# Kernel tuning notes

Measured on AMD Instinct MI355X. Metric: run time of the kernel, lower is better.

Reference implementation:

```python
import jax, jax.numpy as jnp
import numpy as np

NUM_HEADS = 8
QK_DIM = 64
V_DIM = 64


def _conv1x1(W, b, x):
    # W: [out, in], x: [N, in, T, V] -> [N, out, T, V]
    return jnp.einsum('oc,nctv->notv', W, x) + b[None, :, None, None]


def setup_inputs() -> dict:
    key = jax.random.key(0)
    ks = jax.random.split(key, 10)
    N, C, T, V = 8, 256, 1024, 25
    s = 0.02
    return {
        'feature': jax.random.normal(ks[0], (N, C, T, V), jnp.float32),
        'text_feature': jax.random.normal(ks[1], (1, 512, 1, V), jnp.float32),
        'Wq': jax.random.normal(ks[2], (NUM_HEADS * QK_DIM, 512), jnp.float32) * s,
        'bq': jax.random.normal(ks[3], (NUM_HEADS * QK_DIM,), jnp.float32) * s,
        'Wk': jax.random.normal(ks[4], (NUM_HEADS * QK_DIM, 512), jnp.float32) * s,
        'bk': jax.random.normal(ks[5], (NUM_HEADS * QK_DIM,), jnp.float32) * s,
        'Wv': jax.random.normal(ks[6], (V_DIM, C), jnp.float32) * s,
        'bv': jax.random.normal(ks[7], (V_DIM,), jnp.float32) * s,
        'Wo': jax.random.normal(ks[8], (C, NUM_HEADS * V_DIM), jnp.float32) * s,
        'bo': jax.random.normal(ks[9], (C,), jnp.float32) * s,
    }


def reference(feature, text_feature, Wq, bq, Wk, bk, Wv, bv, Wo, bo):
    N, C, T, V = feature.shape
    tf = jnp.broadcast_to(text_feature, (N, 512, 1, V))  # expand over batch
    # Q/K from text features (T dim collapses to 1)
    q = _conv1x1(Wq, bq, tf).reshape(N, NUM_HEADS, QK_DIM, V)
    k = _conv1x1(Wk, bk, tf).reshape(N, NUM_HEADS, QK_DIM, V)
    v = _conv1x1(Wv, bv, feature)  # [N, v_dim, T, V]
    energy = jnp.einsum('nhcu,nhcv->nhuv', q, k) / jnp.sqrt(jnp.float32(QK_DIM))
    attn = jax.nn.softmax(energy, axis=-1)  # [N, H, V, V]
    z = jnp.einsum('nctu,nhuv->nhctv', v, attn).reshape(N, NUM_HEADS * V_DIM, T, V)
    out = _conv1x1(Wo, bo, z) + feature
    return out
```

## Files before the change

kernel.cpp:

```cpp
#include <hip/hip_runtime.h>
#include <hip/hip_bf16.h>


typedef __attribute__((ext_vector_type(8))) short short8;
typedef __attribute__((ext_vector_type(4))) short short4v;
typedef __attribute__((ext_vector_type(4))) float f4v;

static __device__ __forceinline__ unsigned short f2bf(float f) {
  union { float f; unsigned u; } v; v.f = f;
  unsigned r = v.u + 0x7fffu + ((v.u >> 16) & 1u);
  return (unsigned short)(r >> 16);
}
static __device__ __forceinline__ float bf2f(unsigned short h) {
  union { unsigned u; float f; } v; v.u = ((unsigned)h) << 16;
  return v.f;
}


__global__ void k_qk_conv(const float* __restrict__ tf,
                          const float* __restrict__ Wq, const float* __restrict__ bq,
                          const float* __restrict__ Wk, const float* __restrict__ bk,
                          const float* __restrict__ Wv, const float* __restrict__ Wo,
                          unsigned short* __restrict__ WvP,
                          unsigned short* __restrict__ WoP,
                          float* __restrict__ qkP)
{
  __shared__ float tfl[12800];
  const int b = blockIdx.x, tid = threadIdx.x;
  if (b < 100) {
    for (int i = tid; i < 12800; i += 256) tfl[i] = tf[i];
    __syncthreads();
    int idx = b * 256 + tid;
    int isK = idx >= 12800;
    int j = isK ? idx - 12800 : idx;
    int g = j / 25, u = j - 25 * g;
    const float* wrow = (isK ? Wk : Wq) + g * 512;
    float s = (isK ? bk : bq)[g];
    for (int i = 0; i < 512; ++i) s += wrow[i] * tfl[i * 25 + u];
    qkP[idx] = s;
  } else {
    int cb = b - 100;
    for (int i = cb * 256 + tid; i < 16384; i += 64 * 256) {
      WvP[i] = f2bf(Wv[i]);
    }
    for (int i = cb * 256 + tid; i < 131072; i += 64 * 256) {
      WoP[i] = f2bf(Wo[i]);
    }
  }
}

__global__ void k_attn(const float* __restrict__ qkP,
                       unsigned short* __restrict__ attnP)
{
  __shared__ float ql[1600], kl[1600], attl[625];
  const int h = blockIdx.x, tid = threadIdx.x;
  for (int i = tid; i < 1600; i += 256) {
    ql[i] = qkP[h * 1600 + i];
    kl[i] = qkP[12800 + h * 1600 + i];
  }
  __syncthreads();
  if (tid < 25) {
    int u = tid;
    float e[25];
    float mx = -1e30f;
    #pragma unroll
    for (int v = 0; v < 25; ++v) {
      float s = 0.f;
      #pragma unroll
      for (int r = 0; r < 64; ++r) s += ql[r * 25 + u] * kl[r * 25 + v];
      s *= 0.125f;
      e[v] = s;
      mx = fmaxf(mx, s);
    }
    float den = 0.f;
    #pragma unroll
    for (int v = 0; v < 25; ++v) { e[v] = __expf(e[v] - mx); den += e[v]; }
    float inv = 1.f / den;
    #pragma unroll
    for (int v = 0; v < 25; ++v) attl[u * 25 + v] = e[v] * inv;
  }
  __syncthreads();
  for (int i = tid; i < 1280; i += 256) {
    int vp = i / 40, u = i - 40 * vp;
    attnP[h * 1280 + i] =
        (vp < 25 && u < 25) ? f2bf(attl[u * 25 + vp]) : (unsigned short)0;
  }
}

__launch_bounds__(512, 4)
__global__ void k_main(const float* __restrict__ feature,
                       const float* __restrict__ bv,
                       const float* __restrict__ bo,
                       const unsigned short* __restrict__ WvP,
                       const unsigned short* __restrict__ WoP,
                       const unsigned short* __restrict__ attnP,
                       float* __restrict__ out)
{
  extern __shared__ char smem[];
  unsigned short* Fl = (unsigned short*)smem;
  unsigned short* Zl = (unsigned short*)smem;
  unsigned short* Vl = (unsigned short*)(smem + 66560);

  const int tid  = threadIdx.x;
  const int wave = tid >> 6;
  const int lane = tid & 63;
  const int quad = lane >> 4;
  const int l16  = lane & 15;
  const int n  = blockIdx.x & 7;
  const int tb = blockIdx.x >> 3;
  const int t0 = tb * 2;

  if (tid < 462) {
    short8 z = {0, 0, 0, 0, 0, 0, 0, 0};
    int pc = tid / 33, off = tid - 33 * pc;
    int t = pc / 7, vp = 25 + (pc - 7 * t);
    *reinterpret_cast<short8*>(&Fl[(t * 32 + vp) * 264 + off * 8]) = z;
  }

  {
    const int c = tid >> 1, p = tid & 1;
    const float2* src = reinterpret_cast<const float2*>(
        feature + ((size_t)(n * 256 + c) * 1024 + t0) * 25);
    for (int i = p; i < 25; i += 2) {
      float2 f = src[i];
      int j0 = 2 * i;
      {
        int j = j0;       int t = (j >= 25); int vp = j - 25 * t;
        Fl[(t * 32 + vp) * 264 + c] = f2bf(f.x);
      }
      {
        int j = j0 + 1;   int t = (j >= 25); int vp = j - 25 * t;
        Fl[(t * 32 + vp) * 264 + c] = f2bf(f.y);
      }
    }
  }

  const int mt1 = wave & 3, nh1 = wave >> 2;
  short8 wa[8];
  #pragma unroll
  for (int ks = 0; ks < 8; ++ks)
    wa[ks] = *reinterpret_cast<const short8*>(
        WvP + (mt1 * 16 + l16) * 256 + ks * 32 + quad * 8);

  __syncthreads();

  f4v acc[2][4];
  #pragma unroll
  for (int mi = 0; mi < 2; ++mi) {
    const int o0 = wave * 32 + mi * 16 + quad * 4;
    float bo4[4];
    #pragma unroll
    for (int r = 0; r < 4; ++r) bo4[r] = bo[o0 + r];
    #pragma unroll
    for (int ni = 0; ni < 4; ++ni) {
      short4v fr = *reinterpret_cast<const short4v*>(
          &Fl[(ni * 16 + l16) * 264 + o0]);
      #pragma unroll
      for (int r = 0; r < 4; ++r)
        acc[mi][ni][r] = bo4[r] + bf2f((unsigned short)fr[r]);
    }
  }

  {
    f4v accv[2];
    #pragma unroll
    for (int ni = 0; ni < 2; ++ni) {
      #pragma unroll
      for (int r = 0; r < 4; ++r) accv[ni][r] = bv[mt1 * 16 + quad * 4 + r];
    }
    #pragma unroll
    for (int ks = 0; ks < 8; ++ks) {
      #pragma unroll
      for (int ni = 0; ni < 2; ++ni) {
        int colb = (2 * nh1 + ni) * 16 + l16;
        short8 b = *reinterpret_cast<const short8*>(
            &Fl[colb * 264 + ks * 32 + quad * 8]);
        accv[ni] = __builtin_amdgcn_mfma_f32_16x16x32_bf16(wa[ks], b, accv[ni], 0, 0, 0);
      }
    }
    #pragma unroll
    for (int ni = 0; ni < 2; ++ni) {
      int colb = (2 * nh1 + ni) * 16 + l16;
      #pragma unroll
      for (int r = 0; r < 4; ++r) {
        int c = mt1 * 16 + quad * 4 + r;
        Vl[c * 72 + colb] = f2bf(accv[ni][r]);
      }
    }
  }

  const int t2 = wave >> 2, q2 = wave & 3;
  short8 ab[4];
  #pragma unroll
  for (int nj = 0; nj < 4; ++nj) {
    int h = 2 * q2 + (nj >> 1), vph = nj & 1;
    ab[nj] = *reinterpret_cast<const short8*>(
        attnP + h * 1280 + (vph * 16 + l16) * 40 + quad * 8);
  }

  __syncthreads();

  #pragma unroll
  for (int mi = 0; mi < 4; ++mi) {
    short8 a = *reinterpret_cast<const short8*>(
        &Vl[(mi * 16 + l16) * 72 + t2 * 32 + quad * 8]);
    #pragma unroll
    for (int nj = 0; nj < 4; ++nj) {
      f4v z = {0.f, 0.f, 0.f, 0.f};
      f4v accz = __builtin_amdgcn_mfma_f32_16x16x32_bf16(a, ab[nj], z, 0, 0, 0);
      int h = 2 * q2 + (nj >> 1), vph = nj & 1;
      int col = t2 * 32 + vph * 16 + l16;
      int k0 = h * 64 + mi * 16 + quad * 4;
      short4v zz;
      #pragma unroll
      for (int r = 0; r < 4; ++r) zz[r] = (short)f2bf(accz[r]);
      *reinterpret_cast<short4v*>(&Zl[col * 520 + k0]) = zz;
    }
  }

  short8 af01[2][2];
  #pragma unroll
  for (int pk = 0; pk < 2; ++pk)
    #pragma unroll
    for (int mi = 0; mi < 2; ++mi)
      af01[pk][mi] = *reinterpret_cast<const short8*>(
          WoP + (wave * 32 + mi * 16 + l16) * 512 + pk * 32 + quad * 8);

  __syncthreads();

  #pragma unroll
  for (int ks = 0; ks < 16; ++ks) {
    short8 bfr[4], afr[2];
    #pragma unroll
    for (int ni = 0; ni < 4; ++ni)
      bfr[ni] = *reinterpret_cast<const short8*>(
          &Zl[(ni * 16 + l16) * 520 + ks * 32 + quad * 8]);
    if (ks < 2) {
      afr[0] = af01[ks][0];
      afr[1] = af01[ks][1];
    } else {
      #pragma unroll
      for (int mi = 0; mi < 2; ++mi)
        afr[mi] = *reinterpret_cast<const short8*>(
            WoP + (wave * 32 + mi * 16 + l16) * 512 + ks * 32 + quad * 8);
    }
    #pragma unroll
    for (int mi = 0; mi < 2; ++mi) {
      #pragma unroll
      for (int ni = 0; ni < 4; ++ni)
        acc[mi][ni] =
            __builtin_amdgcn_mfma_f32_16x16x32_bf16(afr[mi], bfr[ni], acc[mi][ni], 0, 0, 0);
    }
  }

  #pragma unroll
  for (int ni = 0; ni < 4; ++ni) {
    int colb = ni * 16 + l16;
    int t = colb >> 5, vp = colb & 31;
    if (vp < 25) {
      #pragma unroll
      for (int mi = 0; mi < 2; ++mi) {
        #pragma unroll
        for (int r = 0; r < 4; ++r) {
          int o = wave * 32 + mi * 16 + quad * 4 + r;
          out[((size_t)(n * 256 + o) * 1024 + (t0 + t)) * 25 + vp] = acc[mi][ni][r];
        }
      }
    }
  }
}

extern "C" void kernel_launch(void* const* d_in, const int* in_sizes, int n_in,
                              void* d_out, int out_size, void* d_ws, size_t ws_size,
                              hipStream_t stream)
{
  const float* feature = (const float*)d_in[0];
  const float* tf      = (const float*)d_in[1];
  const float* Wq      = (const float*)d_in[2];
  const float* bq      = (const float*)d_in[3];
  const float* Wk      = (const float*)d_in[4];
  const float* bk      = (const float*)d_in[5];
  const float* Wv      = (const float*)d_in[6];
  const float* bv      = (const float*)d_in[7];
  const float* Wo      = (const float*)d_in[8];
  const float* bo      = (const float*)d_in[9];
  float* out = (float*)d_out;

  unsigned short* WvP   = (unsigned short*)d_ws;
  unsigned short* WoP   = WvP + 16384;
  unsigned short* attnP = WoP + 131072;
  float* qkP = (float*)(attnP + 10240);

  hipLaunchKernelGGL(k_qk_conv, dim3(164), dim3(256), 0, stream,
                     tf, Wq, bq, Wk, bk, Wv, Wo, WvP, WoP, qkP);
  hipLaunchKernelGGL(k_attn, dim3(8), dim3(256), 0, stream, qkP, attnP);

  hipFuncSetAttribute(reinterpret_cast<const void*>(&k_main),
                      hipFuncAttributeMaxDynamicSharedMemorySize, 75776);
  hipLaunchKernelGGL(k_main, dim3(4096), dim3(512), 75776, stream,
                     feature, bv, bo, WvP, WoP, attnP, out);
}
```

Measured before the change: 547.7 us.

## Make main kernel loop over time chunks with double-buffered feature prefetch

The main kernel now launches 256 workgroups, each looping over 16 two-frame tiles of one batch instead of one tile per workgroup. The next tile's feature data is prefetched into registers while the current tile is computed, then written into an alternate LDS buffer. The full Wo fragment set is held in registers for the whole loop rather than reloaded per tile, and outputs use nontemporal stores. In exchange, LDS grows to about 140 KB so only one workgroup fits per CU, the launch bound drops to 2, and register pressure rises, all of which cut the number of waves available to hide latency.

```diff
diff --git a/kernel.cpp b/kernel.cpp
--- a/kernel.cpp
+++ b/kernel.cpp
@@ -87,7 +87,7 @@
   }
 }
 
-__launch_bounds__(512, 4)
+__launch_bounds__(512, 2)
 __global__ void k_main(const float* __restrict__ feature,
                        const float* __restrict__ bv,
                        const float* __restrict__ bo,
@@ -97,43 +97,30 @@
                        float* __restrict__ out)
 {
   extern __shared__ char smem[];
-  unsigned short* Fl = (unsigned short*)smem;
-  unsigned short* Zl = (unsigned short*)smem;
-  unsigned short* Vl = (unsigned short*)(smem + 66560);
+  unsigned short* FlA = (unsigned short*)smem;
+  unsigned short* FlB = (unsigned short*)(smem + 33792);
+  unsigned short* Vl  = (unsigned short*)(smem + 67584);
+  unsigned short* Zl  = (unsigned short*)(smem + 76800);
 
   const int tid  = threadIdx.x;
   const int wave = tid >> 6;
   const int lane = tid & 63;
   const int quad = lane >> 4;
   const int l16  = lane & 15;
-  const int n  = blockIdx.x & 7;
-  const int tb = blockIdx.x >> 3;
-  const int t0 = tb * 2;
-
-  if (tid < 462) {
-    short8 z = {0, 0, 0, 0, 0, 0, 0, 0};
-    int pc = tid / 33, off = tid - 33 * pc;
-    int t = pc / 7, vp = 25 + (pc - 7 * t);
-    *reinterpret_cast<short8*>(&Fl[(t * 32 + vp) * 264 + off * 8]) = z;
-  }
-
-  {
-    const int c = tid >> 1, p = tid & 1;
-    const float2* src = reinterpret_cast<const float2*>(
-        feature + ((size_t)(n * 256 + c) * 1024 + t0) * 25);
-    for (int i = p; i < 25; i += 2) {
-      float2 f = src[i];
-      int j0 = 2 * i;
-      {
-        int j = j0;       int t = (j >= 25); int vp = j - 25 * t;
-        Fl[(t * 32 + vp) * 264 + c] = f2bf(f.x);
-      }
-      {
-        int j = j0 + 1;   int t = (j >= 25); int vp = j - 25 * t;
-        Fl[(t * 32 + vp) * 264 + c] = f2bf(f.y);
-      }
-    }
-  }
+  const int wg    = blockIdx.x;
+  const int n     = wg >> 5;
+  const int chunk = wg & 31;
+
+  const int c = tid >> 1, p = tid & 1;
+  const size_t rowbase = ((size_t)(n * 256 + c) * 1024) * 25;
+
+  short8 wo[2][16];
+  #pragma unroll
+  for (int mi = 0; mi < 2; ++mi)
+    #pragma unroll
+    for (int ks = 0; ks < 16; ++ks)
+      wo[mi][ks] = *reinterpret_cast<const short8*>(
+          WoP + (wave * 32 + mi * 16 + l16) * 512 + ks * 32 + quad * 8);
 
   const int mt1 = wave & 3, nh1 = wave >> 2;
   short8 wa[8];
@@ -141,53 +128,6 @@
   for (int ks = 0; ks < 8; ++ks)
     wa[ks] = *reinterpret_cast<const short8*>(
         WvP + (mt1 * 16 + l16) * 256 + ks * 32 + quad * 8);
-
-  __syncthreads();
-
-  f4v acc[2][4];
-  #pragma unroll
-  for (int mi = 0; mi < 2; ++mi) {
-    const int o0 = wave * 32 + mi * 16 + quad * 4;
-    float bo4[4];
-    #pragma unroll
-    for (int r = 0; r < 4; ++r) bo4[r] = bo[o0 + r];
-    #pragma unroll
-    for (int ni = 0; ni < 4; ++ni) {
-      short4v fr = *reinterpret_cast<const short4v*>(
-          &Fl[(ni * 16 + l16) * 264 + o0]);
-      #pragma unroll
-      for (int r = 0; r < 4; ++r)
-        acc[mi][ni][r] = bo4[r] + bf2f((unsigned short)fr[r]);
-    }
-  }
-
-  {
-    f4v accv[2];
-    #pragma unroll
-    for (int ni = 0; ni < 2; ++ni) {
-      #pragma unroll
-      for (int r = 0; r < 4; ++r) accv[ni][r] = bv[mt1 * 16 + quad * 4 + r];
-    }
-    #pragma unroll
-    for (int ks = 0; ks < 8; ++ks) {
-      #pragma unroll
-      for (int ni = 0; ni < 2; ++ni) {
-        int colb = (2 * nh1 + ni) * 16 + l16;
-        short8 b = *reinterpret_cast<const short8*>(
-            &Fl[colb * 264 + ks * 32 + quad * 8]);
-        accv[ni] = __builtin_amdgcn_mfma_f32_16x16x32_bf16(wa[ks], b, accv[ni], 0, 0, 0);
-      }
-    }
-    #pragma unroll
-    for (int ni = 0; ni < 2; ++ni) {
-      int colb = (2 * nh1 + ni) * 16 + l16;
-      #pragma unroll
-      for (int r = 0; r < 4; ++r) {
-        int c = mt1 * 16 + quad * 4 + r;
-        Vl[c * 72 + colb] = f2bf(accv[ni][r]);
-      }
-    }
-  }
 
   const int t2 = wave >> 2, q2 = wave & 3;
   short8 ab[4];
@@ -198,75 +138,161 @@
         attnP + h * 1280 + (vph * 16 + l16) * 40 + quad * 8);
   }
 
+  float bo4[2][4];
+  #pragma unroll
+  for (int mi = 0; mi < 2; ++mi)
+    #pragma unroll
+    for (int r = 0; r < 4; ++r) bo4[mi][r] = bo[wave * 32 + mi * 16 + quad * 4 + r];
+  float bvv[4];
+  #pragma unroll
+  for (int r = 0; r < 4; ++r) bvv[r] = bv[mt1 * 16 + quad * 4 + r];
+
+  {
+    short8 z = {0, 0, 0, 0, 0, 0, 0, 0};
+    for (int i = tid; i < 924; i += 512) {
+      int pc = i / 33, off = i - 33 * pc;
+      unsigned short* F = (pc < 14) ? FlA : FlB;
+      int r = (pc < 14) ? pc : pc - 14;
+      int t = r / 7, vp = 25 + (r - 7 * t);
+      *reinterpret_cast<short8*>(&F[(t * 32 + vp) * 264 + off * 8]) = z;
+    }
+  }
+
+  float2 fn[13];
+  {
+    const float2* s2 = reinterpret_cast<const float2*>(
+        feature + rowbase + (size_t)(chunk * 32) * 25);
+    #pragma unroll
+    for (int j = 0; j < 13; ++j) { int i = p + 2 * j; if (i < 25) fn[j] = s2[i]; }
+  }
+  #pragma unroll
+  for (int j = 0; j < 13; ++j) {
+    int i = p + 2 * j;
+    if (i < 25) {
+      int j0 = 2 * i;
+      { int jj = j0;     int t = (jj >= 25); int vp = jj - 25 * t; FlA[(t*32+vp)*264 + c] = f2bf(fn[j].x); }
+      { int jj = j0 + 1; int t = (jj >= 25); int vp = jj - 25 * t; FlA[(t*32+vp)*264 + c] = f2bf(fn[j].y); }
+    }
+  }
   __syncthreads();
 
-  #pragma unroll
-  for (int mi = 0; mi < 4; ++mi) {
-    short8 a = *reinterpret_cast<const short8*>(
-        &Vl[(mi * 16 + l16) * 72 + t2 * 32 + quad * 8]);
-    #pragma unroll
-    for (int nj = 0; nj < 4; ++nj) {
-      f4v z = {0.f, 0.f, 0.f, 0.f};
-      f4v accz = __builtin_amdgcn_mfma_f32_16x16x32_bf16(a, ab[nj], z, 0, 0, 0);
-      int h = 2 * q2 + (nj >> 1), vph = nj & 1;
-      int col = t2 * 32 + vph * 16 + l16;
-      int k0 = h * 64 + mi * 16 + quad * 4;
-      short4v zz;
-      #pragma unroll
-      for (int r = 0; r < 4; ++r) zz[r] = (short)f2bf(accz[r]);
-      *reinterpret_cast<short4v*>(&Zl[col * 520 + k0]) = zz;
-    }
-  }
-
-  short8 af01[2][2];
-  #pragma unroll
-  for (int pk = 0; pk < 2; ++pk)
-    #pragma unroll
-    for (int mi = 0; mi < 2; ++mi)
-      af01[pk][mi] = *reinterpret_cast<const short8*>(
-          WoP + (wave * 32 + mi * 16 + l16) * 512 + pk * 32 + quad * 8);
-
-  __syncthreads();
-
-  #pragma unroll
-  for (int ks = 0; ks < 16; ++ks) {
-    short8 bfr[4], afr[2];
-    #pragma unroll
-    for (int ni = 0; ni < 4; ++ni)
-      bfr[ni] = *reinterpret_cast<const short8*>(
-          &Zl[(ni * 16 + l16) * 520 + ks * 32 + quad * 8]);
-    if (ks < 2) {
-      afr[0] = af01[ks][0];
-      afr[1] = af01[ks][1];
-    } else {
+  #pragma unroll 1
+  for (int it = 0; it < 16; ++it) {
+    unsigned short* Fc  = (it & 1) ? FlB : FlA;
+    unsigned short* Fnx = (it & 1) ? FlA : FlB;
+    const int t0 = chunk * 32 + it * 2;
+
+    if (it < 15) {
+      const float2* s2 = reinterpret_cast<const float2*>(
+          feature + rowbase + (size_t)(t0 + 2) * 25);
+      #pragma unroll
+      for (int j = 0; j < 13; ++j) { int i = p + 2 * j; if (i < 25) fn[j] = s2[i]; }
+      __builtin_amdgcn_sched_barrier(0);
+    }
+
+    f4v acc[2][4];
+    #pragma unroll
+    for (int mi = 0; mi < 2; ++mi) {
+      const int o0 = wave * 32 + mi * 16 + quad * 4;
+      #pragma unroll
+      for (int ni = 0; ni < 4; ++ni) {
+        short4v fr = *reinterpret_cast<const short4v*>(&Fc[(ni * 16 + l16) * 264 + o0]);
+        #pragma unroll
+        for (int r = 0; r < 4; ++r)
+          acc[mi][ni][r] = bo4[mi][r] + bf2f((unsigned short)fr[r]);
+      }
+    }
+
+    {
+      f4v accv[2];
+      #pragma unroll
+      for (int ni = 0; ni < 2; ++ni)
+        #pragma unroll
+        for (int r = 0; r < 4; ++r) accv[ni][r] = bvv[r];
+      #pragma unroll
+      for (int ks = 0; ks < 8; ++ks) {
+        #pragma unroll
+        for (int ni = 0; ni < 2; ++ni) {
+          int colb = (2 * nh1 + ni) * 16 + l16;
+          short8 b = *reinterpret_cast<const short8*>(&Fc[colb * 264 + ks * 32 + quad * 8]);
+          accv[ni] = __builtin_amdgcn_mfma_f32_16x16x32_bf16(wa[ks], b, accv[ni], 0, 0, 0);
+        }
+      }
+      #pragma unroll
+      for (int ni = 0; ni < 2; ++ni) {
+        int colb = (2 * nh1 + ni) * 16 + l16;
+        #pragma unroll
+        for (int r = 0; r < 4; ++r) {
+          int cc = mt1 * 16 + quad * 4 + r;
+          Vl[cc * 72 + colb] = f2bf(accv[ni][r]);
+        }
+      }
+    }
+    __syncthreads();
+
+    #pragma unroll
+    for (int mi = 0; mi < 4; ++mi) {
+      short8 a = *reinterpret_cast<const short8*>(
+          &Vl[(mi * 16 + l16) * 72 + t2 * 32 + quad * 8]);
+      #pragma unroll
+      for (int nj = 0; nj < 4; ++nj) {
+        f4v z = {0.f, 0.f, 0.f, 0.f};
+        f4v az = __builtin_amdgcn_mfma_f32_16x16x32_bf16(a, ab[nj], z, 0, 0, 0);
+        int h = 2 * q2 + (nj >> 1), vph = nj & 1;
+        int col = t2 * 32 + vph * 16 + l16;
+        int k0 = h * 64 + mi * 16 + quad * 4;
+        short4v zz;
+        #pragma unroll
+        for (int r = 0; r < 4; ++r) zz[r] = (short)f2bf(az[r]);
+        *reinterpret_cast<short4v*>(&Zl[col * 520 + k0]) = zz;
+      }
+    }
+    __syncthreads();
+
+    #pragma unroll
+    for (int ks = 0; ks < 16; ++ks) {
+      short8 bfr[4];
+      #pragma unroll
+      for (int ni = 0; ni < 4; ++ni)
+        bfr[ni] = *reinterpret_cast<const short8*>(
+            &Zl[(ni * 16 + l16) * 520 + ks * 32 + quad * 8]);
       #pragma unroll
       for (int mi = 0; mi < 2; ++mi)
-        afr[mi] = *reinterpret_cast<const short8*>(
-            WoP + (wave * 32 + mi * 16 + l16) * 512 + ks * 32 + quad * 8);
-    }
-    #pragma unroll
-    for (int mi = 0; mi < 2; ++mi) {
-      #pragma unroll
-      for (int ni = 0; ni < 4; ++ni)
-        acc[mi][ni] =
-            __builtin_amdgcn_mfma_f32_16x16x32_bf16(afr[mi], bfr[ni], acc[mi][ni], 0, 0, 0);
-    }
-  }
-
-  #pragma unroll
-  for (int ni = 0; ni < 4; ++ni) {
-    int colb = ni * 16 + l16;
-    int t = colb >> 5, vp = colb & 31;
-    if (vp < 25) {
-      #pragma unroll
-      for (int mi = 0; mi < 2; ++mi) {
-        #pragma unroll
-        for (int r = 0; r < 4; ++r) {
-          int o = wave * 32 + mi * 16 + quad * 4 + r;
-          out[((size_t)(n * 256 + o) * 1024 + (t0 + t)) * 25 + vp] = acc[mi][ni][r];
+        #pragma unroll
+        for (int ni = 0; ni < 4; ++ni)
+          acc[mi][ni] =
+              __builtin_amdgcn_mfma_f32_16x16x32_bf16(wo[mi][ks], bfr[ni], acc[mi][ni], 0, 0, 0);
+    }
+
+    #pragma unroll
+    for (int ni = 0; ni < 4; ++ni) {
+      int colb = ni * 16 + l16;
+      int t = colb >> 5, vp = colb & 31;
+      if (vp < 25) {
+        #pragma unroll
+        for (int mi = 0; mi < 2; ++mi)
+          #pragma unroll
+          for (int r = 0; r < 4; ++r) {
+            int o = wave * 32 + mi * 16 + quad * 4 + r;
+            __builtin_nontemporal_store(
+                acc[mi][ni][r],
+                &out[((size_t)(n * 256 + o) * 1024 + (t0 + t)) * 25 + vp]);
+          }
+      }
+    }
+
+    if (it < 15) {
+      #pragma unroll
+      for (int j = 0; j < 13; ++j) {
+        int i = p + 2 * j;
+        if (i < 25) {
+          int j0 = 2 * i;
+          { int jj = j0;     int t = (jj >= 25); int vp = jj - 25 * t; Fnx[(t*32+vp)*264 + c] = f2bf(fn[j].x); }
+          { int jj = j0 + 1; int t = (jj >= 25); int vp = jj - 25 * t; Fnx[(t*32+vp)*264 + c] = f2bf(fn[j].y); }
         }
       }
     }
+    __syncthreads();
   }
 }
 
@@ -296,7 +322,7 @@
   hipLaunchKernelGGL(k_attn, dim3(8), dim3(256), 0, stream, qkP, attnP);
 
   hipFuncSetAttribute(reinterpret_cast<const void*>(&k_main),
-                      hipFuncAttributeMaxDynamicSharedMemorySize, 75776);
-  hipLaunchKernelGGL(k_main, dim3(4096), dim3(512), 75776, stream,
+                      hipFuncAttributeMaxDynamicSharedMemorySize, 143360);
+  hipLaunchKernelGGL(k_main, dim3(256), dim3(512), 143360, stream,
                      feature, bv, bo, WvP, WoP, attnP, out);
 }
```

New measurement: 653.2 us. +19.3%, slower.

## Split V projection into separate kernel with bf16 workspace, reorganize main kernel per head

Applied to the files above, without the earlier changes.

Moves the Wv 1x1 conv into a new kernel k_vm that writes V in bf16 to a global workspace. k_main then reads V from that workspace, assigns one head per wave for the attention mix, and reads the residual feature in fp32 straight from global memory instead of from the bf16 LDS copy. Wv/Wo weight loads are double-buffered, and LDS per block shrinks. The cost is an extra kernel launch, a V round trip through global memory, and a second read of feature.

```diff
diff --git a/kernel.cpp b/kernel.cpp
--- a/kernel.cpp
+++ b/kernel.cpp
@@ -10,10 +10,6 @@
   union { float f; unsigned u; } v; v.f = f;
   unsigned r = v.u + 0x7fffu + ((v.u >> 16) & 1u);
   return (unsigned short)(r >> 16);
-}
-static __device__ __forceinline__ float bf2f(unsigned short h) {
-  union { unsigned u; float f; } v; v.u = ((unsigned)h) << 16;
-  return v.f;
 }
 
 
@@ -87,169 +83,182 @@
   }
 }
 
-__launch_bounds__(512, 4)
-__global__ void k_main(const float* __restrict__ feature,
-                       const float* __restrict__ bv,
-                       const float* __restrict__ bo,
-                       const unsigned short* __restrict__ WvP,
-                       const unsigned short* __restrict__ WoP,
-                       const unsigned short* __restrict__ attnP,
-                       float* __restrict__ out)
-{
-  extern __shared__ char smem[];
-  unsigned short* Fl = (unsigned short*)smem;
-  unsigned short* Zl = (unsigned short*)smem;
-  unsigned short* Vl = (unsigned short*)(smem + 66560);
-
+__launch_bounds__(256)
+__attribute__((amdgpu_waves_per_eu(4, 4)))
+__global__ void k_vm(const float* __restrict__ feature,
+                     const float* __restrict__ bv,
+                     const unsigned short* __restrict__ WvP,
+                     unsigned short* __restrict__ Vws)
+{
+  __shared__ unsigned short Fl[64 * 264];
   const int tid  = threadIdx.x;
   const int wave = tid >> 6;
   const int lane = tid & 63;
   const int quad = lane >> 4;
   const int l16  = lane & 15;
-  const int n  = blockIdx.x & 7;
-  const int tb = blockIdx.x >> 3;
-  const int t0 = tb * 2;
-
-  if (tid < 462) {
+  const int n    = blockIdx.x & 7;
+  const int tile = blockIdx.x >> 3;
+  const int t0   = tile * 2;
+
+  {
     short8 z = {0, 0, 0, 0, 0, 0, 0, 0};
-    int pc = tid / 33, off = tid - 33 * pc;
-    int t = pc / 7, vp = 25 + (pc - 7 * t);
-    *reinterpret_cast<short8*>(&Fl[(t * 32 + vp) * 264 + off * 8]) = z;
+    for (int i = tid; i < 448; i += 256) {
+      int pc = i >> 5, off = i & 31;
+      int t = pc / 7, vp = 25 + (pc - 7 * t);
+      *reinterpret_cast<short8*>(&Fl[(t * 32 + vp) * 264 + off * 8]) = z;
+    }
   }
 
   {
-    const int c = tid >> 1, p = tid & 1;
-    const float2* src = reinterpret_cast<const float2*>(
+    const int c = tid;
+    const float2* s2 = reinterpret_cast<const float2*>(
         feature + ((size_t)(n * 256 + c) * 1024 + t0) * 25);
-    for (int i = p; i < 25; i += 2) {
-      float2 f = src[i];
-      int j0 = 2 * i;
-      {
-        int j = j0;       int t = (j >= 25); int vp = j - 25 * t;
-        Fl[(t * 32 + vp) * 264 + c] = f2bf(f.x);
+    float2 buf[13];
+    #pragma unroll
+    for (int j = 0; j < 13; ++j) buf[j] = s2[j];
+    #pragma unroll
+    for (int j = 0; j < 13; ++j) {
+      int f0 = 2 * j;
+      { int t = f0 / 25, vp = f0 - 25 * t;  Fl[(t * 32 + vp) * 264 + c] = f2bf(buf[j].x); }
+      { int f1 = f0 + 1; int t = f1 / 25, vp = f1 - 25 * t;
+        Fl[(t * 32 + vp) * 264 + c] = f2bf(buf[j].y); }
+    }
+    #pragma unroll
+    for (int j = 0; j < 12; ++j) buf[j] = s2[13 + j];
+    #pragma unroll
+    for (int j = 0; j < 12; ++j) {
+      int f0 = 26 + 2 * j;
+      { int t = f0 / 25, vp = f0 - 25 * t;  Fl[(t * 32 + vp) * 264 + c] = f2bf(buf[j].x); }
+      { int f1 = f0 + 1; int t = f1 / 25, vp = f1 - 25 * t;
+        Fl[(t * 32 + vp) * 264 + c] = f2bf(buf[j].y); }
+    }
+  }
+  __syncthreads();
+
+  const unsigned short* wvb = WvP + (wave * 16 + l16) * 256 + quad * 8;
+  f4v acc[4];
+  #pragma unroll
+  for (int r = 0; r < 4; ++r) {
+    float b = bv[wave * 16 + quad * 4 + r];
+    #pragma unroll
+    for (int ni = 0; ni < 4; ++ni) acc[ni][r] = b;
+  }
+  short8 wap[2];
+  wap[0] = *reinterpret_cast<const short8*>(wvb);
+  wap[1] = *reinterpret_cast<const short8*>(wvb + 32);
+  #pragma unroll
+  for (int ks = 0; ks < 8; ++ks) {
+    short8 a = wap[ks & 1];
+    if (ks < 6)
+      wap[ks & 1] = *reinterpret_cast<const short8*>(wvb + (ks + 2) * 32);
+    #pragma unroll
+    for (int ni = 0; ni < 4; ++ni) {
+      short8 b = *reinterpret_cast<const short8*>(
+          &Fl[(ni * 16 + l16) * 264 + ks * 32 + quad * 8]);
+      acc[ni] = __builtin_amdgcn_mfma_f32_16x16x32_bf16(a, b, acc[ni], 0, 0, 0);
+    }
+  }
+
+  #pragma unroll
+  for (int ni = 0; ni < 4; ++ni) {
+    int col = ni * 16 + l16;
+    int t = col >> 5, u = col & 31;
+    unsigned short* dst = Vws + ((size_t)(n * 1024 + t0 + t) * 64) * 32 + u;
+    #pragma unroll
+    for (int r = 0; r < 4; ++r)
+      dst[(wave * 16 + quad * 4 + r) * 32] = f2bf(acc[ni][r]);
+  }
+}
+
+__launch_bounds__(512)
+__attribute__((amdgpu_waves_per_eu(4, 4)))
+__global__ void k_main(const float* __restrict__ feature,
+                       const float* __restrict__ bo,
+                       const unsigned short* __restrict__ WoP,
+                       const unsigned short* __restrict__ attnP,
+                       const unsigned short* __restrict__ Vws,
+                       float* __restrict__ out)
+{
+  extern __shared__ char smem[];
+  unsigned short* Zl = (unsigned short*)smem;
+
+  const int tid  = threadIdx.x;
+  const int wave = tid >> 6;
+  const int lane = tid & 63;
+  const int quad = lane >> 4;
+  const int l16  = lane & 15;
+  const int n    = blockIdx.x & 7;
+  const int tile = blockIdx.x >> 3;
+  const int t0   = tile * 2;
+  const int h    = wave;
+
+  short8 ab[2];
+  #pragma unroll
+  for (int vt = 0; vt < 2; ++vt)
+    ab[vt] = *reinterpret_cast<const short8*>(
+        attnP + h * 1280 + (vt * 16 + l16) * 40 + quad * 8);
+
+  const unsigned short* vbase =
+      Vws + ((size_t)(n * 1024 + t0) * 64) * 32 + quad * 8;
+  #pragma unroll
+  for (int ct = 0; ct < 4; ++ct) {
+    #pragma unroll
+    for (int t = 0; t < 2; ++t) {
+      short8 a = *reinterpret_cast<const short8*>(
+          vbase + (size_t)t * 2048 + (ct * 16 + l16) * 32);
+      #pragma unroll
+      for (int vt = 0; vt < 2; ++vt) {
+        f4v z0 = {0.f, 0.f, 0.f, 0.f};
+        f4v az = __builtin_amdgcn_mfma_f32_16x16x32_bf16(a, ab[vt], z0, 0, 0, 0);
+        int col = t * 32 + vt * 16 + l16;
+        int k0 = h * 64 + ct * 16 + quad * 4;
+        short4v zz;
+        #pragma unroll
+        for (int r = 0; r < 4; ++r) zz[r] = (short)f2bf(az[r]);
+        *reinterpret_cast<short4v*>(&Zl[col * 520 + k0]) = zz;
       }
-      {
-        int j = j0 + 1;   int t = (j >= 25); int vp = j - 25 * t;
-        Fl[(t * 32 + vp) * 264 + c] = f2bf(f.y);
-      }
-    }
-  }
-
-  const int mt1 = wave & 3, nh1 = wave >> 2;
-  short8 wa[8];
-  #pragma unroll
-  for (int ks = 0; ks < 8; ++ks)
-    wa[ks] = *reinterpret_cast<const short8*>(
-        WvP + (mt1 * 16 + l16) * 256 + ks * 32 + quad * 8);
-
-  __syncthreads();
+    }
+  }
 
   f4v acc[2][4];
   #pragma unroll
   for (int mi = 0; mi < 2; ++mi) {
     const int o0 = wave * 32 + mi * 16 + quad * 4;
-    float bo4[4];
-    #pragma unroll
-    for (int r = 0; r < 4; ++r) bo4[r] = bo[o0 + r];
+    #pragma unroll
+    for (int r = 0; r < 4; ++r) {
+      float bor = bo[o0 + r];
+      const float* frow = feature + ((size_t)(n * 256 + o0 + r) * 1024 + t0) * 25;
+      #pragma unroll
+      for (int ni = 0; ni < 4; ++ni) {
+        int colb = ni * 16 + l16;
+        int t = colb >> 5, vp = colb & 31;
+        float res = (vp < 25) ? frow[t * 25 + vp] : 0.f;
+        acc[mi][ni][r] = bor + res;
+      }
+    }
+  }
+  __syncthreads();
+
+  const unsigned short* wob = WoP + (wave * 32 + l16) * 512 + quad * 8;
+  short8 wop[2][2];
+  wop[0][0] = *reinterpret_cast<const short8*>(wob);
+  wop[0][1] = *reinterpret_cast<const short8*>(wob + 8192);
+  wop[1][0] = *reinterpret_cast<const short8*>(wob + 32);
+  wop[1][1] = *reinterpret_cast<const short8*>(wob + 8192 + 32);
+  #pragma unroll
+  for (int ks = 0; ks < 16; ++ks) {
+    short8 w0 = wop[ks & 1][0];
+    short8 w1 = wop[ks & 1][1];
+    if (ks < 14) {
+      wop[ks & 1][0] = *reinterpret_cast<const short8*>(wob + (ks + 2) * 32);
+      wop[ks & 1][1] = *reinterpret_cast<const short8*>(wob + 8192 + (ks + 2) * 32);
+    }
     #pragma unroll
     for (int ni = 0; ni < 4; ++ni) {
-      short4v fr = *reinterpret_cast<const short4v*>(
-          &Fl[(ni * 16 + l16) * 264 + o0]);
-      #pragma unroll
-      for (int r = 0; r < 4; ++r)
-        acc[mi][ni][r] = bo4[r] + bf2f((unsigned short)fr[r]);
-    }
-  }
-
-  {
-    f4v accv[2];
-    #pragma unroll
-    for (int ni = 0; ni < 2; ++ni) {
-      #pragma unroll
-      for (int r = 0; r < 4; ++r) accv[ni][r] = bv[mt1 * 16 + quad * 4 + r];
-    }
-    #pragma unroll
-    for (int ks = 0; ks < 8; ++ks) {
-      #pragma unroll
-      for (int ni = 0; ni < 2; ++ni) {
-        int colb = (2 * nh1 + ni) * 16 + l16;
-        short8 b = *reinterpret_cast<const short8*>(
-            &Fl[colb * 264 + ks * 32 + quad * 8]);
-        accv[ni] = __builtin_amdgcn_mfma_f32_16x16x32_bf16(wa[ks], b, accv[ni], 0, 0, 0);
-      }
-    }
-    #pragma unroll
-    for (int ni = 0; ni < 2; ++ni) {
-      int colb = (2 * nh1 + ni) * 16 + l16;
-      #pragma unroll
-      for (int r = 0; r < 4; ++r) {
-        int c = mt1 * 16 + quad * 4 + r;
-        Vl[c * 72 + colb] = f2bf(accv[ni][r]);
-      }
-    }
-  }
-
-  const int t2 = wave >> 2, q2 = wave & 3;
-  short8 ab[4];
-  #pragma unroll
-  for (int nj = 0; nj < 4; ++nj) {
-    int h = 2 * q2 + (nj >> 1), vph = nj & 1;
-    ab[nj] = *reinterpret_cast<const short8*>(
-        attnP + h * 1280 + (vph * 16 + l16) * 40 + quad * 8);
-  }
-
-  __syncthreads();
-
-  #pragma unroll
-  for (int mi = 0; mi < 4; ++mi) {
-    short8 a = *reinterpret_cast<const short8*>(
-        &Vl[(mi * 16 + l16) * 72 + t2 * 32 + quad * 8]);
-    #pragma unroll
-    for (int nj = 0; nj < 4; ++nj) {
-      f4v z = {0.f, 0.f, 0.f, 0.f};
-      f4v accz = __builtin_amdgcn_mfma_f32_16x16x32_bf16(a, ab[nj], z, 0, 0, 0);
-      int h = 2 * q2 + (nj >> 1), vph = nj & 1;
-      int col = t2 * 32 + vph * 16 + l16;
-      int k0 = h * 64 + mi * 16 + quad * 4;
-      short4v zz;
-      #pragma unroll
-      for (int r = 0; r < 4; ++r) zz[r] = (short)f2bf(accz[r]);
-      *reinterpret_cast<short4v*>(&Zl[col * 520 + k0]) = zz;
-    }
-  }
-
-  short8 af01[2][2];
-  #pragma unroll
-  for (int pk = 0; pk < 2; ++pk)
-    #pragma unroll
-    for (int mi = 0; mi < 2; ++mi)
-      af01[pk][mi] = *reinterpret_cast<const short8*>(
-          WoP + (wave * 32 + mi * 16 + l16) * 512 + pk * 32 + quad * 8);
-
-  __syncthreads();
-
-  #pragma unroll
-  for (int ks = 0; ks < 16; ++ks) {
-    short8 bfr[4], afr[2];
-    #pragma unroll
-    for (int ni = 0; ni < 4; ++ni)
-      bfr[ni] = *reinterpret_cast<const short8*>(
+      short8 bfr = *reinterpret_cast<const short8*>(
           &Zl[(ni * 16 + l16) * 520 + ks * 32 + quad * 8]);
-    if (ks < 2) {
-      afr[0] = af01[ks][0];
-      afr[1] = af01[ks][1];
-    } else {
-      #pragma unroll
-      for (int mi = 0; mi < 2; ++mi)
-        afr[mi] = *reinterpret_cast<const short8*>(
-            WoP + (wave * 32 + mi * 16 + l16) * 512 + ks * 32 + quad * 8);
-    }
-    #pragma unroll
-    for (int mi = 0; mi < 2; ++mi) {
-      #pragma unroll
-      for (int ni = 0; ni < 4; ++ni)
-        acc[mi][ni] =
-            __builtin_amdgcn_mfma_f32_16x16x32_bf16(afr[mi], bfr[ni], acc[mi][ni], 0, 0, 0);
+      acc[0][ni] = __builtin_amdgcn_mfma_f32_16x16x32_bf16(w0, bfr, acc[0][ni], 0, 0, 0);
+      acc[1][ni] = __builtin_amdgcn_mfma_f32_16x16x32_bf16(w1, bfr, acc[1][ni], 0, 0, 0);
     }
   }
 
@@ -259,13 +268,12 @@
     int t = colb >> 5, vp = colb & 31;
     if (vp < 25) {
       #pragma unroll
-      for (int mi = 0; mi < 2; ++mi) {
+      for (int mi = 0; mi < 2; ++mi)
         #pragma unroll
         for (int r = 0; r < 4; ++r) {
           int o = wave * 32 + mi * 16 + quad * 4 + r;
           out[((size_t)(n * 256 + o) * 1024 + (t0 + t)) * 25 + vp] = acc[mi][ni][r];
         }
-      }
     }
   }
 }
@@ -290,13 +298,17 @@
   unsigned short* WoP   = WvP + 16384;
   unsigned short* attnP = WoP + 131072;
   float* qkP = (float*)(attnP + 10240);
+  unsigned short* Vws   = (unsigned short*)(qkP + 25600);
 
   hipLaunchKernelGGL(k_qk_conv, dim3(164), dim3(256), 0, stream,
                      tf, Wq, bq, Wk, bk, Wv, Wo, WvP, WoP, qkP);
   hipLaunchKernelGGL(k_attn, dim3(8), dim3(256), 0, stream, qkP, attnP);
 
+  hipLaunchKernelGGL(k_vm, dim3(4096), dim3(256), 0, stream,
+                     feature, bv, WvP, Vws);
+
   hipFuncSetAttribute(reinterpret_cast<const void*>(&k_main),
-                      hipFuncAttributeMaxDynamicSharedMemorySize, 75776);
-  hipLaunchKernelGGL(k_main, dim3(4096), dim3(512), 75776, stream,
-                     feature, bv, bo, WvP, WoP, attnP, out);
-}
+                      hipFuncAttributeMaxDynamicSharedMemorySize, 66560);
+  hipLaunchKernelGGL(k_main, dim3(4096), dim3(512), 66560, stream,
+                     feature, bo, WoP, attnP, Vws, out);
+}
```

After: 595.7 us. 1.09x slower.
